# Kernel optimization log

Measured on AMD Instinct MI355X. Metric: run time of the kernel, lower is better.

## Reference

```python
import jax, jax.numpy as jnp
import numpy as np

# 5 standard YOLOv2 anchors (w, h) in grid units
ANCHORS = np.array([[0.57273, 0.677385], [1.87446, 2.06253], [3.33843, 5.47434],
                    [7.88282, 3.52778], [9.77052, 9.16828]], dtype=np.float32)
NA = 5
OBJECT_SCALE = 5.0
NO_OBJECT_SCALE = 1.0
COORD_SCALE = 1.0
SIL_THRESH = 0.6


def bbox_iou(b1, b2):
    """IoU for center-format boxes; b1/b2 are (x, y, w, h) tuples of broadcastable arrays."""
    x1, y1, w1, h1 = b1
    x2, y2, w2, h2 = b2
    mx = jnp.minimum(x1 - w1 * 0.5, x2 - w2 * 0.5)
    Mx = jnp.maximum(x1 + w1 * 0.5, x2 + w2 * 0.5)
    my = jnp.minimum(y1 - h1 * 0.5, y2 - h2 * 0.5)
    My = jnp.maximum(y1 + h1 * 0.5, y2 + h2 * 0.5)
    cw = w1 + w2 - (Mx - mx)  # intersection width
    ch = h1 + h2 - (My - my)  # intersection height
    carea = jnp.where((cw <= 0) | (ch <= 0), 0.0, cw * ch)
    uarea = w1 * h1 + w2 * h2 - carea
    return carea / uarea


def setup_inputs() -> dict:
    key = jax.random.key(0)
    k1, k2 = jax.random.split(key)
    pred = jax.random.normal(k1, (512, NA * 5, 76, 76), dtype=jnp.float32)
    # normalized gt boxes in (0,1); clip so grid indices stay in range and w,h > 0
    target = jnp.clip(jax.random.uniform(k2, (512, 4), dtype=jnp.float32), 1e-3, 0.999)
    return {"pred": pred, "target": target}


def reference(pred, target):
    bs, _, H, W = pred.shape  # H == W asserted in original
    dt = pred.dtype
    pred = pred.reshape(bs, NA, 5, H, W)
    anc = jnp.asarray(ANCHORS)

    # activations (pred_boxes: sigmoid on x,y; raw w,h; sigmoid conf)
    sx = jax.nn.sigmoid(pred[:, :, 0])
    sy = jax.nn.sigmoid(pred[:, :, 1])
    pw = pred[:, :, 2]
    ph = pred[:, :, 3]
    pconf = jax.nn.sigmoid(pred[:, :, 4])

    # grid-offset boxes (detached in original)
    gj_grid, gi_grid = jnp.meshgrid(jnp.arange(H, dtype=dt), jnp.arange(W, dtype=dt), indexing='ij')
    bx = jax.lax.stop_gradient(sx) + gi_grid
    by = jax.lax.stop_gradient(sy) + gj_grid
    bw = jnp.exp(jax.lax.stop_gradient(pw)) * anc[:, 0].reshape(1, NA, 1, 1)
    bh = jnp.exp(jax.lax.stop_gradient(ph)) * anc[:, 1].reshape(1, NA, 1, 1)

    tgt = jax.lax.stop_gradient(target)
    gx = tgt[:, 0] * W
    gy = tgt[:, 1] * H
    gw = tgt[:, 2] * W
    gh = tgt[:, 3] * H

    # conf mask: no_object_scale everywhere, 0 where IoU(gt, pred) > sil_thresh
    bc = lambda v: v.reshape(bs, 1, 1, 1)
    iou_all = bbox_iou((bc(gx), bc(gy), bc(gw), bc(gh)), (bx, by, bw, bh))  # (bs, NA, H, W)
    conf_mask = jnp.where(iou_all > SIL_THRESH, 0.0, NO_OBJECT_SCALE).astype(dt)

    # best anchor per batch element (wh-only IoU at origin)
    z_b = jnp.zeros((bs, 1), dt)
    z_a = jnp.zeros((1, NA), dt)
    iou_anc = bbox_iou((z_b, z_b, gw[:, None], gh[:, None]),
                       (z_a, z_a, anc[None, :, 0], anc[None, :, 1]))  # (bs, NA)
    best = jnp.argmax(iou_anc, axis=1)

    gi = gx.astype(jnp.int32)
    gj = gy.astype(jnp.int32)
    bidx = jnp.arange(bs)

    # IoU between gt and the matched predicted box
    pb = (bx[bidx, best, gj, gi], by[bidx, best, gj, gi],
          bw[bidx, best, gj, gi], bh[bidx, best, gj, gi])
    iou_t = bbox_iou((gx, gy, gw, gh), pb)

    # scatter target assignment (epoch == 0 branch of original: coord_mask=1, xy target base 0.5)
    conf_mask = conf_mask.at[bidx, best, gj, gi].set(OBJECT_SCALE)
    coord_mask = jnp.ones((bs, NA, H, W), dt)
    bahw = (bs, NA, H, W)
    tb_x = jnp.full(bahw, 0.5, dt).at[bidx, best, gj, gi].set(gx - gi.astype(dt))
    tb_y = jnp.full(bahw, 0.5, dt).at[bidx, best, gj, gi].set(gy - gj.astype(dt))
    tb_w = jnp.zeros(bahw, dt).at[bidx, best, gj, gi].set(jnp.log(gw / anc[best, 0]))
    tb_h = jnp.zeros(bahw, dt).at[bidx, best, gj, gi].set(jnp.log(gh / anc[best, 1]))
    tconf = jnp.zeros(bahw, dt).at[bidx, best, gj, gi].set(iou_t)

    cm = jnp.sqrt(conf_mask)
    sse = lambda a, b: jnp.sum((a - b) ** 2)
    loss_x = COORD_SCALE * sse(sx * coord_mask, tb_x * coord_mask) / 2.0
    loss_y = COORD_SCALE * sse(sy * coord_mask, tb_y * coord_mask) / 2.0
    loss_w = COORD_SCALE * sse(pw * coord_mask, tb_w * coord_mask) / 2.0
    loss_h = COORD_SCALE * sse(ph * coord_mask, tb_h * coord_mask) / 2.0
    loss_conf = sse(pconf * cm, tconf * cm) / 2.0
    loss = loss_x + loss_y + loss_w + loss_h + loss_conf
    return (loss, loss_x, loss_y, loss_w, loss_h, loss_conf)
```

## Files before the change

kernel.cpp:

```cpp
#include <hip/hip_runtime.h>
#include <math.h>

#define NA 5
#define HH 76
#define WW 76
#define HWSZ (HH * WW)
#define HW4 (HWSZ / 4)
#define NBLK (512 * NA)
#define OBJECT_SCALE 5.0f
#define SIL_THRESH 0.6f

#define REC_OFF 16
#define REC_STRIDE 12
#define PART_OFF 8192

__constant__ float ANC_W[NA] = {0.57273f, 1.87446f, 3.33843f, 7.88282f, 9.77052f};
__constant__ float ANC_H[NA] = {0.677385f, 2.06253f, 5.47434f, 3.52778f, 9.16828f};

typedef float v4f __attribute__((ext_vector_type(4)));

__global__ void prep_kernel(const float* __restrict__ target, float* __restrict__ ws, int bs) {
    int b = threadIdx.x;
    if (b >= bs) return;
    float gx = target[b * 4 + 0] * (float)WW;
    float gy = target[b * 4 + 1] * (float)HH;
    float gw = target[b * 4 + 2] * (float)WW;
    float gh = target[b * 4 + 3] * (float)HH;
    int best = 0;
    float bestv = -1.0f;
#pragma unroll
    for (int a = 0; a < NA; ++a) {
        float aw = ANC_W[a], ah = ANC_H[a];
        float inter = fminf(gw, aw) * fminf(gh, ah);
        float uni = gw * gh + aw * ah - inter;
        float iou = inter / uni;
        if (iou > bestv) { bestv = iou; best = a; }
    }
    int gi = (int)gx;
    int gj = (int)gy;
    float* r = ws + REC_OFF + b * REC_STRIDE;
    r[0] = gx; r[1] = gy; r[2] = gw; r[3] = gh;
    r[4] = gx - (float)gi;
    r[5] = gy - (float)gj;
    r[6] = logf(gw / ANC_W[best]);
    r[7] = logf(gh / ANC_H[best]);
    ((int*)r)[8] = best;
    ((int*)r)[9] = gi;
    ((int*)r)[10] = gj;
}

__device__ __forceinline__ float sigmoidf_fast(float x) {
    return 1.0f / (1.0f + __expf(-x));
}

__global__ __launch_bounds__(256) void
region_loss_main(const float* __restrict__ pred, float* __restrict__ ws) {
    const int ba = blockIdx.x;
    const int b  = ba / NA;
    const int a  = ba - b * NA;

    const float* rec = ws + REC_OFF + b * REC_STRIDE;
    const float gx = rec[0], gy = rec[1], gw = rec[2], gh = rec[3];
    const float tx_s = rec[4], ty_s = rec[5], tw_s = rec[6], th_s = rec[7];
    const int best = ((const int*)rec)[8];
    const int gi   = ((const int*)rec)[9];
    const int gj   = ((const int*)rec)[10];
    const float anw = ANC_W[a], anh = ANC_H[a];
    const bool anchit = (a == best);
    const float gxm = gx - gw * 0.5f, gxM = gx + gw * 0.5f;
    const float gym = gy - gh * 0.5f, gyM = gy + gh * 0.5f;
    const float garea = gw * gh;

    const float* base = pred + (size_t)ba * 5 * HWSZ;
    float ax = 0.f, ay = 0.f, aw_ = 0.f, ah_ = 0.f, ac = 0.f;

    for (int r = threadIdx.x; r < HW4; r += 256) {
        const int e0 = r * 4;
        const int j  = r / 19;
        const int i0 = e0 - j * WW;

        v4f px = __builtin_nontemporal_load((const v4f*)(base + e0));
        v4f py = __builtin_nontemporal_load((const v4f*)(base + HWSZ + e0));
        v4f pw = __builtin_nontemporal_load((const v4f*)(base + 2 * HWSZ + e0));
        v4f ph = __builtin_nontemporal_load((const v4f*)(base + 3 * HWSZ + e0));
        v4f pc = __builtin_nontemporal_load((const v4f*)(base + 4 * HWSZ + e0));

        const bool rowhit = anchit && (j == gj) && (gi >= i0) && (gi < i0 + 4);

#pragma unroll
        for (int k = 0; k < 4; ++k) {
            float sx = sigmoidf_fast(px[k]);
            float sy = sigmoidf_fast(py[k]);
            float sc = sigmoidf_fast(pc[k]);
            float bw = __expf(pw[k]) * anw;
            float bh = __expf(ph[k]) * anh;
            float bx = sx + (float)(i0 + k);
            float by = sy + (float)j;
            float mx = fminf(gxm, bx - bw * 0.5f);
            float Mx = fmaxf(gxM, bx + bw * 0.5f);
            float my = fminf(gym, by - bh * 0.5f);
            float My = fmaxf(gyM, by + bh * 0.5f);
            float cw = gw + bw - (Mx - mx);
            float ch = gh + bh - (My - my);
            float carea = (cw <= 0.f || ch <= 0.f) ? 0.f : cw * ch;
            float uarea = garea + bw * bh - carea;
            float iou = carea / uarea;

            float cmask = (iou > SIL_THRESH) ? 0.f : 1.f;
            float tx = 0.5f, ty = 0.5f, tw = 0.f, th = 0.f, tconf = 0.f;
            if (rowhit && (i0 + k) == gi) {
                cmask = OBJECT_SCALE;
                tx = tx_s; ty = ty_s; tw = tw_s; th = th_s;
                tconf = iou;
            }
            float dx = sx - tx, dy = sy - ty;
            float dw = pw[k] - tw, dh = ph[k] - th;
            float dc = sc - tconf;
            ax += dx * dx;
            ay += dy * dy;
            aw_ += dw * dw;
            ah_ += dh * dh;
            ac += cmask * dc * dc;
        }
    }

    __shared__ float sred[4][5];
    int lane = threadIdx.x & 63;
    int wid  = threadIdx.x >> 6;
    float vals[5] = {ax, ay, aw_, ah_, ac};
#pragma unroll
    for (int v = 0; v < 5; ++v) {
        float x = vals[v];
#pragma unroll
        for (int off = 32; off > 0; off >>= 1) x += __shfl_down(x, off, 64);
        if (lane == 0) sred[wid][v] = x;
    }
    __syncthreads();
    if (threadIdx.x < 5) {
        float s = sred[0][threadIdx.x] + sred[1][threadIdx.x] +
                  sred[2][threadIdx.x] + sred[3][threadIdx.x];
        ws[PART_OFF + blockIdx.x * 8 + threadIdx.x] = s;
    }
}

__global__ __launch_bounds__(256) void
reduce_finish(const float* __restrict__ ws, float* __restrict__ out) {
    float s0 = 0.f, s1 = 0.f, s2 = 0.f, s3 = 0.f, s4 = 0.f;
    for (int i = threadIdx.x; i < NBLK; i += 256) {
        const float* p = ws + PART_OFF + i * 8;
        s0 += p[0]; s1 += p[1]; s2 += p[2]; s3 += p[3]; s4 += p[4];
    }
    __shared__ float sred[4][5];
    int lane = threadIdx.x & 63;
    int wid  = threadIdx.x >> 6;
    float vals[5] = {s0, s1, s2, s3, s4};
#pragma unroll
    for (int v = 0; v < 5; ++v) {
        float x = vals[v];
#pragma unroll
        for (int off = 32; off > 0; off >>= 1) x += __shfl_down(x, off, 64);
        if (lane == 0) sred[wid][v] = x;
    }
    __syncthreads();
    if (threadIdx.x == 0) {
        float lx = (sred[0][0] + sred[1][0] + sred[2][0] + sred[3][0]) * 0.5f;
        float ly = (sred[0][1] + sred[1][1] + sred[2][1] + sred[3][1]) * 0.5f;
        float lw = (sred[0][2] + sred[1][2] + sred[2][2] + sred[3][2]) * 0.5f;
        float lh = (sred[0][3] + sred[1][3] + sred[2][3] + sred[3][3]) * 0.5f;
        float lc = (sred[0][4] + sred[1][4] + sred[2][4] + sred[3][4]) * 0.5f;
        out[0] = lx + ly + lw + lh + lc;
        out[1] = lx;
        out[2] = ly;
        out[3] = lw;
        out[4] = lh;
        out[5] = lc;
    }
}

extern "C" void kernel_launch(void* const* d_in, const int* in_sizes, int n_in,
                              void* d_out, int out_size, void* d_ws, size_t ws_size,
                              hipStream_t stream) {
    const float* pred   = (const float*)d_in[0];
    const float* target = (const float*)d_in[1];
    float* ws  = (float*)d_ws;
    float* out = (float*)d_out;
    int bs = in_sizes[1] / 4;

    prep_kernel<<<1, 512, 0, stream>>>(target, ws, bs);
    region_loss_main<<<bs * NA, 256, 0, stream>>>(pred, ws);
    reduce_finish<<<1, 256, 0, stream>>>(ws, out);
}
```

Measured before the change: 378.8 us.

## Flatten main loop to grid-stride over all pred vec4s with per-channel work

Replaces the one-block-per-(batch,anchor) layout with a fixed grid of 2048 blocks that grid-stride over every float4 of the prediction tensor. Coord channels compute their own squared error from a single load, while conf-channel threads reload the four coord planes to compute IoU, so the coord planes are read twice (the second read possibly from cache). Nontemporal loads are dropped in favour of plain loads. The intent is better load balance and occupancy, at the cost of redundant reads, per-element integer divisions and warp divergence across channel types.

```diff
diff --git a/kernel.cpp b/kernel.cpp
--- a/kernel.cpp
+++ b/kernel.cpp
@@ -6,7 +6,9 @@
 #define WW 76
 #define HWSZ (HH * WW)
 #define HW4 (HWSZ / 4)
-#define NBLK (512 * NA)
+#define PLANES (512 * NA * 5)
+#define TOT4 (PLANES * HW4)
+#define GMAIN 2048
 #define OBJECT_SCALE 5.0f
 #define SIL_THRESH 0.6f
 
@@ -55,72 +57,82 @@
 
 __global__ __launch_bounds__(256) void
 region_loss_main(const float* __restrict__ pred, float* __restrict__ ws) {
-    const int ba = blockIdx.x;
-    const int b  = ba / NA;
-    const int a  = ba - b * NA;
-
-    const float* rec = ws + REC_OFF + b * REC_STRIDE;
-    const float gx = rec[0], gy = rec[1], gw = rec[2], gh = rec[3];
-    const float tx_s = rec[4], ty_s = rec[5], tw_s = rec[6], th_s = rec[7];
-    const int best = ((const int*)rec)[8];
-    const int gi   = ((const int*)rec)[9];
-    const int gj   = ((const int*)rec)[10];
-    const float anw = ANC_W[a], anh = ANC_H[a];
-    const bool anchit = (a == best);
-    const float gxm = gx - gw * 0.5f, gxM = gx + gw * 0.5f;
-    const float gym = gy - gh * 0.5f, gyM = gy + gh * 0.5f;
-    const float garea = gw * gh;
-
-    const float* base = pred + (size_t)ba * 5 * HWSZ;
     float ax = 0.f, ay = 0.f, aw_ = 0.f, ah_ = 0.f, ac = 0.f;
 
-    for (int r = threadIdx.x; r < HW4; r += 256) {
-        const int e0 = r * 4;
+    for (int idx = blockIdx.x * 256 + threadIdx.x; idx < TOT4; idx += GMAIN * 256) {
+        const int p  = idx / HW4;
+        const int r  = idx - p * HW4;
+        const int ba = p / 5;
+        const int c  = p - ba * 5;
+        const int b  = ba / 5;
+        const int a  = ba - b * 5;
         const int j  = r / 19;
-        const int i0 = e0 - j * WW;
-
-        v4f px = __builtin_nontemporal_load((const v4f*)(base + e0));
-        v4f py = __builtin_nontemporal_load((const v4f*)(base + HWSZ + e0));
-        v4f pw = __builtin_nontemporal_load((const v4f*)(base + 2 * HWSZ + e0));
-        v4f ph = __builtin_nontemporal_load((const v4f*)(base + 3 * HWSZ + e0));
-        v4f pc = __builtin_nontemporal_load((const v4f*)(base + 4 * HWSZ + e0));
-
-        const bool rowhit = anchit && (j == gj) && (gi >= i0) && (gi < i0 + 4);
-
-#pragma unroll
-        for (int k = 0; k < 4; ++k) {
-            float sx = sigmoidf_fast(px[k]);
-            float sy = sigmoidf_fast(py[k]);
-            float sc = sigmoidf_fast(pc[k]);
-            float bw = __expf(pw[k]) * anw;
-            float bh = __expf(ph[k]) * anh;
-            float bx = sx + (float)(i0 + k);
-            float by = sy + (float)j;
-            float mx = fminf(gxm, bx - bw * 0.5f);
-            float Mx = fmaxf(gxM, bx + bw * 0.5f);
-            float my = fminf(gym, by - bh * 0.5f);
-            float My = fmaxf(gyM, by + bh * 0.5f);
-            float cw = gw + bw - (Mx - mx);
-            float ch = gh + bh - (My - my);
-            float carea = (cw <= 0.f || ch <= 0.f) ? 0.f : cw * ch;
-            float uarea = garea + bw * bh - carea;
-            float iou = carea / uarea;
-
-            float cmask = (iou > SIL_THRESH) ? 0.f : 1.f;
-            float tx = 0.5f, ty = 0.5f, tw = 0.f, th = 0.f, tconf = 0.f;
-            if (rowhit && (i0 + k) == gi) {
-                cmask = OBJECT_SCALE;
-                tx = tx_s; ty = ty_s; tw = tw_s; th = th_s;
-                tconf = iou;
+        const int i0 = (r - j * 19) * 4;
+
+        const float* rec = ws + REC_OFF + b * REC_STRIDE;
+        const int best = ((const int*)rec)[8];
+        const int gi   = ((const int*)rec)[9];
+        const int gj   = ((const int*)rec)[10];
+        const bool rowhit = (a == best) && (j == gj) && (gi >= i0) && (gi < i0 + 4);
+
+        const float* self = pred + (size_t)idx * 4;
+        v4f v = *(const v4f*)self;
+
+        if (c < 4) {
+            const float ts  = rec[4 + c];
+            const float def = (c < 2) ? 0.5f : 0.0f;
+            float acc = 0.f;
+#pragma unroll
+            for (int k = 0; k < 4; ++k) {
+                float s = (c < 2) ? sigmoidf_fast(v[k]) : v[k];
+                float t = (rowhit && (i0 + k) == gi) ? ts : def;
+                float d = s - t;
+                acc += d * d;
             }
-            float dx = sx - tx, dy = sy - ty;
-            float dw = pw[k] - tw, dh = ph[k] - th;
-            float dc = sc - tconf;
-            ax += dx * dx;
-            ay += dy * dy;
-            aw_ += dw * dw;
-            ah_ += dh * dh;
-            ac += cmask * dc * dc;
+            if (c == 0) ax += acc;
+            else if (c == 1) ay += acc;
+            else if (c == 2) aw_ += acc;
+            else ah_ += acc;
+        } else {
+            const float gx = rec[0], gy = rec[1], gw = rec[2], gh = rec[3];
+            const float anw = ANC_W[a], anh = ANC_H[a];
+            const float gxm = gx - gw * 0.5f, gxM = gx + gw * 0.5f;
+            const float gym = gy - gh * 0.5f, gyM = gy + gh * 0.5f;
+            const float garea = gw * gh;
+
+            const float* cb = self - 4 * HWSZ;
+            v4f px = *(const v4f*)(cb);
+            v4f py = *(const v4f*)(cb + HWSZ);
+            v4f pw = *(const v4f*)(cb + 2 * HWSZ);
+            v4f ph = *(const v4f*)(cb + 3 * HWSZ);
+#pragma unroll
+            for (int k = 0; k < 4; ++k) {
+                float sx = sigmoidf_fast(px[k]);
+                float sy = sigmoidf_fast(py[k]);
+                float sc = sigmoidf_fast(v[k]);
+                float bw = __expf(pw[k]) * anw;
+                float bh = __expf(ph[k]) * anh;
+                float bx = sx + (float)(i0 + k);
+                float by = sy + (float)j;
+                float mx = fminf(gxm, bx - bw * 0.5f);
+                float Mx = fmaxf(gxM, bx + bw * 0.5f);
+                float my = fminf(gym, by - bh * 0.5f);
+                float My = fmaxf(gyM, by + bh * 0.5f);
+                float cw = gw + bw - (Mx - mx);
+                float ch = gh + bh - (My - my);
+                float carea = (cw <= 0.f || ch <= 0.f) ? 0.f : cw * ch;
+                float uarea = garea + bw * bh - carea;
+                float iou = carea / uarea;
+
+                float cmask = (iou > SIL_THRESH) ? 0.f : 1.f;
+                float tconf = 0.f;
+                if (rowhit && (i0 + k) == gi) {
+                    cmask = OBJECT_SCALE;
+                    tconf = iou;
+                }
+                float dc = sc - tconf;
+                ac += cmask * dc * dc;
+            }
         }
     }
 
@@ -129,11 +141,11 @@
     int wid  = threadIdx.x >> 6;
     float vals[5] = {ax, ay, aw_, ah_, ac};
 #pragma unroll
-    for (int v = 0; v < 5; ++v) {
-        float x = vals[v];
+    for (int vv = 0; vv < 5; ++vv) {
+        float x = vals[vv];
 #pragma unroll
         for (int off = 32; off > 0; off >>= 1) x += __shfl_down(x, off, 64);
-        if (lane == 0) sred[wid][v] = x;
+        if (lane == 0) sred[wid][vv] = x;
     }
     __syncthreads();
     if (threadIdx.x < 5) {
@@ -146,7 +158,7 @@
 __global__ __launch_bounds__(256) void
 reduce_finish(const float* __restrict__ ws, float* __restrict__ out) {
     float s0 = 0.f, s1 = 0.f, s2 = 0.f, s3 = 0.f, s4 = 0.f;
-    for (int i = threadIdx.x; i < NBLK; i += 256) {
+    for (int i = threadIdx.x; i < GMAIN; i += 256) {
         const float* p = ws + PART_OFF + i * 8;
         s0 += p[0]; s1 += p[1]; s2 += p[2]; s3 += p[3]; s4 += p[4];
     }
@@ -187,6 +199,6 @@
     int bs = in_sizes[1] / 4;
 
     prep_kernel<<<1, 512, 0, stream>>>(target, ws, bs);
-    region_loss_main<<<bs * NA, 256, 0, stream>>>(pred, ws);
+    region_loss_main<<<GMAIN, 256, 0, stream>>>(pred, ws);
     reduce_finish<<<1, 256, 0, stream>>>(ws, out);
 }
```

Result: slower. 405.7 us (+7.1%).
